# Performance work log

Hardware: AMD Instinct MI355X
Metric: run time of the kernel (lower is better)

## Reference

```python
import jax, jax.numpy as jnp
import numpy as np

B, T, D, H = 2, 2048, 1024, 16
DH = D // H


def setup_inputs() -> dict:
    key = jax.random.key(0)
    ks = jax.random.split(key, 5)
    s = 1.0 / np.sqrt(D)
    return {
        "x": jax.random.normal(ks[0], (B, T, D), dtype=jnp.float32),
        "Wq": jax.random.normal(ks[1], (D, D), dtype=jnp.float32) * s,
        "Wk": jax.random.normal(ks[2], (D, D), dtype=jnp.float32) * s,
        "Wv": jax.random.normal(ks[3], (D, D), dtype=jnp.float32) * s,
        "Wo": jax.random.normal(ks[4], (D, D), dtype=jnp.float32) * s,
    }


def reference(x, Wq, Wk, Wv, Wo):
    # torch nn.Linear(bias=False): y = x @ W.T, weight shape [out, in]
    q = (x @ Wq.T).reshape(B, T, H, DH).transpose(0, 2, 1, 3)  # [B,H,T,Dh]
    k = (x @ Wk.T).reshape(B, T, H, DH).transpose(0, 2, 1, 3)
    v = (x @ Wv.T).reshape(B, T, H, DH).transpose(0, 2, 1, 3)
    scores = jnp.einsum("bhqd,bhkd->bhqk", q, k) / jnp.sqrt(jnp.float32(DH))
    att = jax.nn.softmax(scores, axis=-1)
    y = jnp.einsum("bhqk,bhkd->bhqd", att, v)  # [B,H,T,Dh]
    y = y.transpose(0, 2, 1, 3).reshape(B, T, D)
    return y @ Wo.T
```

## Files before the change

### kernel.cpp

```cpp
#include <hip/hip_runtime.h>
#include <math.h>

typedef __attribute__((ext_vector_type(8))) _Float16 half8;
typedef __attribute__((ext_vector_type(4))) float f32x4;

namespace {
constexpr int T_ = 2048, DH_ = 64;
constexpr int M_ = 4096;
constexpr int KD = 1024;
}

__global__ __launch_bounds__(256)
void conv_half4(const float* __restrict__ s0, const float* __restrict__ s1,
                const float* __restrict__ s2, const float* __restrict__ s3,
                _Float16* __restrict__ dst)
{
    const float* s = (blockIdx.y == 0) ? s0 : (blockIdx.y == 1) ? s1
                   : (blockIdx.y == 2) ? s2 : s3;
    const size_t i = ((size_t)blockIdx.x * 256 + threadIdx.x) * 8;
    const float4 a = *reinterpret_cast<const float4*>(s + i);
    const float4 b = *reinterpret_cast<const float4*>(s + i + 4);
    half8 h;
    h[0] = (_Float16)a.x; h[1] = (_Float16)a.y; h[2] = (_Float16)a.z; h[3] = (_Float16)a.w;
    h[4] = (_Float16)b.x; h[5] = (_Float16)b.y; h[6] = (_Float16)b.z; h[7] = (_Float16)b.w;
    *reinterpret_cast<half8*>(dst + (size_t)blockIdx.y * 1048576 + i) = h;
}

__global__ __launch_bounds__(256)
void gemm_half(const _Float16* __restrict__ A, const _Float16* __restrict__ Bw,
               float* __restrict__ Cout,
               _Float16* __restrict__ qh, _Float16* __restrict__ kh,
               _Float16* __restrict__ vh, const int mode)
{
    __shared__ _Float16 As[128 * 64];
    __shared__ _Float16 Bs[64 * 64];
    const int tid = threadIdx.x;
    const int l   = tid & 63;
    const int w   = tid >> 6;
    const int wm  = w >> 1, wn = w & 1;
    const int m0  = blockIdx.y * 128;
    const int n0  = blockIdx.x * 64;

    f32x4 acc[4][2];
#pragma unroll
    for (int i = 0; i < 4; ++i)
#pragma unroll
        for (int j = 0; j < 2; ++j) acc[i][j] = (f32x4){0.f, 0.f, 0.f, 0.f};

    const int srow = l >> 3;
    const int scol = ((l & 7) ^ srow) << 3;
    const int frow = l & 15;
    const int fkb  = (l >> 4) << 4;

    for (int kt = 0; kt < 16; ++kt) {
        const int kOff = kt << 6;
#pragma unroll
        for (int s = 0; s < 4; ++s) {
            const int j = (w << 2) + s;
            const _Float16* gp = A + (size_t)(m0 + (j << 3) + srow) * KD + kOff + scol;
            __builtin_amdgcn_global_load_lds(
                (const __attribute__((address_space(1))) void*)gp,
                (__attribute__((address_space(3))) void*)(As + (j << 9)), 16, 0, 0);
        }
#pragma unroll
        for (int s = 0; s < 2; ++s) {
            const int j = (w << 1) + s;
            const _Float16* gp = Bw + (size_t)(n0 + (j << 3) + srow) * KD + kOff + scol;
            __builtin_amdgcn_global_load_lds(
                (const __attribute__((address_space(1))) void*)gp,
                (__attribute__((address_space(3))) void*)(Bs + (j << 9)), 16, 0, 0);
        }
        __syncthreads();
#pragma unroll
        for (int ks = 0; ks < 2; ++ks) {
            half8 af[4], bfr[2];
#pragma unroll
            for (int fi = 0; fi < 4; ++fi) {
                const int row = wm * 64 + fi * 16 + frow;
                const int cb  = (ks * 64 + fkb) ^ ((row & 7) << 4);
                af[fi] = *reinterpret_cast<const half8*>(
                    reinterpret_cast<const char*>(As) + row * 128 + cb);
            }
#pragma unroll
            for (int fj = 0; fj < 2; ++fj) {
                const int row = wn * 32 + fj * 16 + frow;
                const int cb  = (ks * 64 + fkb) ^ ((row & 7) << 4);
                bfr[fj] = *reinterpret_cast<const half8*>(
                    reinterpret_cast<const char*>(Bs) + row * 128 + cb);
            }
#pragma unroll
            for (int fi = 0; fi < 4; ++fi)
#pragma unroll
                for (int fj = 0; fj < 2; ++fj)
                    acc[fi][fj] = __builtin_amdgcn_mfma_f32_16x16x32_f16(
                        af[fi], bfr[fj], acc[fi][fj], 0, 0, 0);
        }
        __syncthreads();
    }

    const int r0 = (l >> 4) << 2;
#pragma unroll
    for (int fi = 0; fi < 4; ++fi)
#pragma unroll
        for (int fj = 0; fj < 2; ++fj)
#pragma unroll
            for (int r = 0; r < 4; ++r) {
                const int m = m0 + wm * 64 + fi * 16 + r0 + r;
                const int n = n0 + wn * 32 + fj * 16 + (l & 15);
                const float vv = acc[fi][fj][r];
                if (mode == 0) {
                    const int bb = m >> 11, t = m & 2047;
                    const int which = n >> 10, nl = n & 1023;
                    const int hh = nl >> 6, dh = nl & 63;
                    const int bh = (bb << 4) + hh;
                    if (which == 0)
                        qh[(((size_t)bh << 11) + t) * 64 + dh] = (_Float16)(vv * 0.125f);
                    else if (which == 1)
                        kh[(((size_t)bh << 11) + t) * 64 + dh] = (_Float16)vv;
                    else
                        vh[(((size_t)bh << 6) + dh) * 2048 + t] = (_Float16)vv;
                } else {
                    Cout[(size_t)m * 1024 + n] = vv;
                }
            }
}

#define SWZ(row, bytecol) (((row) << 7) + ((bytecol) ^ (((row) & 7) << 4)))

__global__ __launch_bounds__(256)
void attn_mfma(const _Float16* __restrict__ Qh, const _Float16* __restrict__ Kh,
               const _Float16* __restrict__ Vh, _Float16* __restrict__ Yh)
{
    __shared__ _Float16 Ks[2][64 * 64];
    __shared__ _Float16 Vs[2][64 * 64];
    __shared__ _Float16 Ps[64 * 64];
    const int tid = threadIdx.x;
    const int l   = tid & 63;
    const int w   = tid >> 6;
    const int g4  = l >> 4;
    const int c16 = l & 15;
    const int bh  = blockIdx.y;
    const int t0  = blockIdx.x * 64;
    const size_t qkbase = (size_t)bh * T_ * DH_;
    const size_t vbase  = (size_t)bh * DH_ * T_;

    const int srow = l >> 3;
    const int scol = ((l & 7) ^ srow) << 3;

    half8 qf[2];
#pragma unroll
    for (int ks = 0; ks < 2; ++ks)
        qf[ks] = *reinterpret_cast<const half8*>(
            Qh + qkbase + (size_t)(t0 + w * 16 + c16) * 64 + ks * 32 + g4 * 8);

    half8 ones;
#pragma unroll
    for (int j = 0; j < 8; ++j) ones[j] = (_Float16)1.f;

#pragma unroll
    for (int s = 0; s < 2; ++s) {
        const int j   = (w << 1) + s;
        const int row = (j << 3) + srow;
        const _Float16* gk = Kh + qkbase + (size_t)row * 64 + scol;
        __builtin_amdgcn_global_load_lds(
            (const __attribute__((address_space(1))) void*)gk,
            (__attribute__((address_space(3))) void*)(&Ks[0][0] + (j << 9)), 16, 0, 0);
        const _Float16* gv = Vh + vbase + (size_t)row * T_ + scol;
        __builtin_amdgcn_global_load_lds(
            (const __attribute__((address_space(1))) void*)gv,
            (__attribute__((address_space(3))) void*)(&Vs[0][0] + (j << 9)), 16, 0, 0);
    }
    __syncthreads();

    f32x4 o[4], ol;
#pragma unroll
    for (int i = 0; i < 4; ++i) o[i] = (f32x4){0.f, 0.f, 0.f, 0.f};
    ol = (f32x4){0.f, 0.f, 0.f, 0.f};

    for (int ktile = 0; ktile < T_ / 64; ++ktile) {
        const int cur = ktile & 1;
        if (ktile + 1 < T_ / 64) {
            const int nxt = cur ^ 1;
#pragma unroll
            for (int s = 0; s < 2; ++s) {
                const int j   = (w << 1) + s;
                const int row = (j << 3) + srow;
                const _Float16* gk = Kh + qkbase +
                    (size_t)((ktile + 1) * 64 + row) * 64 + scol;
                __builtin_amdgcn_global_load_lds(
                    (const __attribute__((address_space(1))) void*)gk,
                    (__attribute__((address_space(3))) void*)(&Ks[nxt][0] + (j << 9)), 16, 0, 0);
                const _Float16* gv = Vh + vbase + (size_t)row * T_ +
                    (ktile + 1) * 64 + scol;
                __builtin_amdgcn_global_load_lds(
                    (const __attribute__((address_space(1))) void*)gv,
                    (__attribute__((address_space(3))) void*)(&Vs[nxt][0] + (j << 9)), 16, 0, 0);
            }
        }

        const char* ksBase = reinterpret_cast<const char*>(&Ks[cur][0]);
        const char* vsBase = reinterpret_cast<const char*>(&Vs[cur][0]);
        f32x4 s[4];
#pragma unroll
        for (int fj = 0; fj < 4; ++fj) s[fj] = (f32x4){0.f, 0.f, 0.f, 0.f};
        __builtin_amdgcn_s_setprio(1);
#pragma unroll
        for (int ks = 0; ks < 2; ++ks)
#pragma unroll
            for (int fj = 0; fj < 4; ++fj) {
                const int row = fj * 16 + c16;
                const half8 kf = *reinterpret_cast<const half8*>(
                    ksBase + SWZ(row, ks * 64 + (g4 << 4)));
                s[fj] = __builtin_amdgcn_mfma_f32_16x16x32_f16(qf[ks], kf, s[fj], 0, 0, 0);
            }
        __builtin_amdgcn_s_setprio(0);

#pragma unroll
        for (int r4 = 0; r4 < 4; ++r4) {
            const int q = w * 16 + (g4 << 2) + r4;
#pragma unroll
            for (int fj = 0; fj < 4; ++fj) {
                const float p = __expf(fminf(s[fj][r4], 11.f));
                *reinterpret_cast<_Float16*>(reinterpret_cast<char*>(Ps) +
                    SWZ(q, fj * 32 + (c16 << 1))) = (_Float16)p;
            }
        }

        __builtin_amdgcn_s_setprio(1);
#pragma unroll
        for (int ks = 0; ks < 2; ++ks) {
            const int prow = w * 16 + c16;
            const half8 pf = *reinterpret_cast<const half8*>(
                reinterpret_cast<const char*>(Ps) + SWZ(prow, ks * 64 + (g4 << 4)));
#pragma unroll
            for (int fj = 0; fj < 4; ++fj) {
                const int vrow = fj * 16 + c16;
                const half8 vf = *reinterpret_cast<const half8*>(
                    vsBase + SWZ(vrow, ks * 64 + (g4 << 4)));
                o[fj] = __builtin_amdgcn_mfma_f32_16x16x32_f16(pf, vf, o[fj], 0, 0, 0);
            }
            ol = __builtin_amdgcn_mfma_f32_16x16x32_f16(pf, ones, ol, 0, 0, 0);
        }
        __builtin_amdgcn_s_setprio(0);

        __syncthreads();
    }

    const int bb = bh >> 4, hh = bh & 15;
#pragma unroll
    for (int r4 = 0; r4 < 4; ++r4) {
        const int t = t0 + w * 16 + (g4 << 2) + r4;
        const float inv = 1.f / ol[r4];
        const size_t mrow = ((size_t)bb * T_ + t) * 1024;
#pragma unroll
        for (int fj = 0; fj < 4; ++fj) {
            const int col = hh * 64 + fj * 16 + c16;
            Yh[mrow + col] = (_Float16)(o[fj][r4] * inv);
        }
    }
}

extern "C" void kernel_launch(void* const* d_in, const int* in_sizes, int n_in,
                              void* d_out, int out_size, void* d_ws, size_t ws_size,
                              hipStream_t stream)
{
    const float* x  = (const float*)d_in[0];
    const float* Wq = (const float*)d_in[1];
    const float* Wk = (const float*)d_in[2];
    const float* Wv = (const float*)d_in[3];
    const float* Wo = (const float*)d_in[4];

    unsigned char* ws = (unsigned char*)d_ws;
    _Float16* xh = (_Float16*)ws;
    _Float16* wh = (_Float16*)(ws + (size_t) 8388608);
    _Float16* qh = (_Float16*)(ws + (size_t)16777216);
    _Float16* kh = (_Float16*)(ws + (size_t)25165824);
    _Float16* vh = (_Float16*)(ws + (size_t)33554432);
    _Float16* yh = xh;

    conv_half4<<<dim3(2048, 1), 256, 0, stream>>>(x, nullptr, nullptr, nullptr, xh);
    conv_half4<<<dim3(512, 4), 256, 0, stream>>>(Wq, Wk, Wv, Wo, wh);

    dim3 blk(256);
    dim3 g1(48, 32);
    gemm_half<<<g1, blk, 0, stream>>>(xh, wh, nullptr, qh, kh, vh, 0);

    dim3 ga(T_ / 64, 32);
    attn_mfma<<<ga, blk, 0, stream>>>(qh, kh, vh, yh);

    dim3 g2(16, 32);
    gemm_half<<<g2, blk, 0, stream>>>(yh, wh + (size_t)3072 * KD, (float*)d_out,
                                      nullptr, nullptr, nullptr, 1);
}
```

Before: 154.7 us.

## Enlarge GEMM N-tile to 128 and give each attention warp 32 query rows

The projection GEMMs now compute 128x128 tiles instead of 128x64, so every A-tile load feeds twice as many MFMAs. The attention kernel processes 128 queries per block, with each warp handling two 16-row groups that share each K/V fragment read from LDS. The softmax scale now folds log2(e) into Q so the kernel can use exp2f, with the overflow clamp adjusted to match. In exchange, register pressure rises and there are fewer blocks: 256 for the out-projection and 512 for attention, which may underfill the GPU's compute units.

```diff
diff --git a/kernel.cpp b/kernel.cpp
--- a/kernel.cpp
+++ b/kernel.cpp
@@ -33,19 +33,19 @@
                _Float16* __restrict__ vh, const int mode)
 {
     __shared__ _Float16 As[128 * 64];
-    __shared__ _Float16 Bs[64 * 64];
+    __shared__ _Float16 Bs[128 * 64];
     const int tid = threadIdx.x;
     const int l   = tid & 63;
     const int w   = tid >> 6;
     const int wm  = w >> 1, wn = w & 1;
     const int m0  = blockIdx.y * 128;
-    const int n0  = blockIdx.x * 64;
-
-    f32x4 acc[4][2];
+    const int n0  = blockIdx.x * 128;
+
+    f32x4 acc[4][4];
 #pragma unroll
     for (int i = 0; i < 4; ++i)
 #pragma unroll
-        for (int j = 0; j < 2; ++j) acc[i][j] = (f32x4){0.f, 0.f, 0.f, 0.f};
+        for (int j = 0; j < 4; ++j) acc[i][j] = (f32x4){0.f, 0.f, 0.f, 0.f};
 
     const int srow = l >> 3;
     const int scol = ((l & 7) ^ srow) << 3;
@@ -63,8 +63,8 @@
                 (__attribute__((address_space(3))) void*)(As + (j << 9)), 16, 0, 0);
         }
 #pragma unroll
-        for (int s = 0; s < 2; ++s) {
-            const int j = (w << 1) + s;
+        for (int s = 0; s < 4; ++s) {
+            const int j = (w << 2) + s;
             const _Float16* gp = Bw + (size_t)(n0 + (j << 3) + srow) * KD + kOff + scol;
             __builtin_amdgcn_global_load_lds(
                 (const __attribute__((address_space(1))) void*)gp,
@@ -73,7 +73,7 @@
         __syncthreads();
 #pragma unroll
         for (int ks = 0; ks < 2; ++ks) {
-            half8 af[4], bfr[2];
+            half8 af[4], bfr[4];
 #pragma unroll
             for (int fi = 0; fi < 4; ++fi) {
                 const int row = wm * 64 + fi * 16 + frow;
@@ -82,8 +82,8 @@
                     reinterpret_cast<const char*>(As) + row * 128 + cb);
             }
 #pragma unroll
-            for (int fj = 0; fj < 2; ++fj) {
-                const int row = wn * 32 + fj * 16 + frow;
+            for (int fj = 0; fj < 4; ++fj) {
+                const int row = wn * 64 + fj * 16 + frow;
                 const int cb  = (ks * 64 + fkb) ^ ((row & 7) << 4);
                 bfr[fj] = *reinterpret_cast<const half8*>(
                     reinterpret_cast<const char*>(Bs) + row * 128 + cb);
@@ -91,7 +91,7 @@
 #pragma unroll
             for (int fi = 0; fi < 4; ++fi)
 #pragma unroll
-                for (int fj = 0; fj < 2; ++fj)
+                for (int fj = 0; fj < 4; ++fj)
                     acc[fi][fj] = __builtin_amdgcn_mfma_f32_16x16x32_f16(
                         af[fi], bfr[fj], acc[fi][fj], 0, 0, 0);
         }
@@ -99,14 +99,15 @@
     }
 
     const int r0 = (l >> 4) << 2;
+    const float QSC = 0.125f * 1.44269504f;
 #pragma unroll
     for (int fi = 0; fi < 4; ++fi)
 #pragma unroll
-        for (int fj = 0; fj < 2; ++fj)
+        for (int fj = 0; fj < 4; ++fj)
 #pragma unroll
             for (int r = 0; r < 4; ++r) {
                 const int m = m0 + wm * 64 + fi * 16 + r0 + r;
-                const int n = n0 + wn * 32 + fj * 16 + (l & 15);
+                const int n = n0 + wn * 64 + fj * 16 + (l & 15);
                 const float vv = acc[fi][fj][r];
                 if (mode == 0) {
                     const int bb = m >> 11, t = m & 2047;
@@ -114,7 +115,7 @@
                     const int hh = nl >> 6, dh = nl & 63;
                     const int bh = (bb << 4) + hh;
                     if (which == 0)
-                        qh[(((size_t)bh << 11) + t) * 64 + dh] = (_Float16)(vv * 0.125f);
+                        qh[(((size_t)bh << 11) + t) * 64 + dh] = (_Float16)(vv * QSC);
                     else if (which == 1)
                         kh[(((size_t)bh << 11) + t) * 64 + dh] = (_Float16)vv;
                     else
@@ -133,25 +134,28 @@
 {
     __shared__ _Float16 Ks[2][64 * 64];
     __shared__ _Float16 Vs[2][64 * 64];
-    __shared__ _Float16 Ps[64 * 64];
+    __shared__ _Float16 Ps[128 * 64];
     const int tid = threadIdx.x;
     const int l   = tid & 63;
     const int w   = tid >> 6;
     const int g4  = l >> 4;
     const int c16 = l & 15;
     const int bh  = blockIdx.y;
-    const int t0  = blockIdx.x * 64;
+    const int t0  = blockIdx.x * 128;
     const size_t qkbase = (size_t)bh * T_ * DH_;
     const size_t vbase  = (size_t)bh * DH_ * T_;
 
     const int srow = l >> 3;
     const int scol = ((l & 7) ^ srow) << 3;
 
-    half8 qf[2];
-#pragma unroll
-    for (int ks = 0; ks < 2; ++ks)
-        qf[ks] = *reinterpret_cast<const half8*>(
-            Qh + qkbase + (size_t)(t0 + w * 16 + c16) * 64 + ks * 32 + g4 * 8);
+    half8 qf[2][2];
+#pragma unroll
+    for (int ri = 0; ri < 2; ++ri)
+#pragma unroll
+        for (int ks = 0; ks < 2; ++ks)
+            qf[ri][ks] = *reinterpret_cast<const half8*>(
+                Qh + qkbase + (size_t)(t0 + w * 32 + ri * 16 + c16) * 64
+                    + ks * 32 + g4 * 8);
 
     half8 ones;
 #pragma unroll
@@ -172,10 +176,13 @@
     }
     __syncthreads();
 
-    f32x4 o[4], ol;
-#pragma unroll
-    for (int i = 0; i < 4; ++i) o[i] = (f32x4){0.f, 0.f, 0.f, 0.f};
-    ol = (f32x4){0.f, 0.f, 0.f, 0.f};
+    f32x4 o[2][4], ol[2];
+#pragma unroll
+    for (int ri = 0; ri < 2; ++ri) {
+#pragma unroll
+        for (int i = 0; i < 4; ++i) o[ri][i] = (f32x4){0.f, 0.f, 0.f, 0.f};
+        ol[ri] = (f32x4){0.f, 0.f, 0.f, 0.f};
+    }
 
     for (int ktile = 0; ktile < T_ / 64; ++ktile) {
         const int cur = ktile & 1;
@@ -200,9 +207,11 @@
 
         const char* ksBase = reinterpret_cast<const char*>(&Ks[cur][0]);
         const char* vsBase = reinterpret_cast<const char*>(&Vs[cur][0]);
-        f32x4 s[4];
-#pragma unroll
-        for (int fj = 0; fj < 4; ++fj) s[fj] = (f32x4){0.f, 0.f, 0.f, 0.f};
+        f32x4 s[2][4];
+#pragma unroll
+        for (int ri = 0; ri < 2; ++ri)
+#pragma unroll
+            for (int fj = 0; fj < 4; ++fj) s[ri][fj] = (f32x4){0.f, 0.f, 0.f, 0.f};
         __builtin_amdgcn_s_setprio(1);
 #pragma unroll
         for (int ks = 0; ks < 2; ++ks)
@@ -211,35 +220,41 @@
                 const int row = fj * 16 + c16;
                 const half8 kf = *reinterpret_cast<const half8*>(
                     ksBase + SWZ(row, ks * 64 + (g4 << 4)));
-                s[fj] = __builtin_amdgcn_mfma_f32_16x16x32_f16(qf[ks], kf, s[fj], 0, 0, 0);
+                s[0][fj] = __builtin_amdgcn_mfma_f32_16x16x32_f16(qf[0][ks], kf, s[0][fj], 0, 0, 0);
+                s[1][fj] = __builtin_amdgcn_mfma_f32_16x16x32_f16(qf[1][ks], kf, s[1][fj], 0, 0, 0);
             }
         __builtin_amdgcn_s_setprio(0);
 
 #pragma unroll
-        for (int r4 = 0; r4 < 4; ++r4) {
-            const int q = w * 16 + (g4 << 2) + r4;
-#pragma unroll
-            for (int fj = 0; fj < 4; ++fj) {
-                const float p = __expf(fminf(s[fj][r4], 11.f));
-                *reinterpret_cast<_Float16*>(reinterpret_cast<char*>(Ps) +
-                    SWZ(q, fj * 32 + (c16 << 1))) = (_Float16)p;
-            }
-        }
+        for (int ri = 0; ri < 2; ++ri)
+#pragma unroll
+            for (int r4 = 0; r4 < 4; ++r4) {
+                const int q = w * 32 + ri * 16 + (g4 << 2) + r4;
+#pragma unroll
+                for (int fj = 0; fj < 4; ++fj) {
+                    const float p = exp2f(fminf(s[ri][fj][r4], 15.9f));
+                    *reinterpret_cast<_Float16*>(reinterpret_cast<char*>(Ps) +
+                        SWZ(q, fj * 32 + (c16 << 1))) = (_Float16)p;
+                }
+            }
 
         __builtin_amdgcn_s_setprio(1);
 #pragma unroll
         for (int ks = 0; ks < 2; ++ks) {
-            const int prow = w * 16 + c16;
-            const half8 pf = *reinterpret_cast<const half8*>(
-                reinterpret_cast<const char*>(Ps) + SWZ(prow, ks * 64 + (g4 << 4)));
+            const half8 pf0 = *reinterpret_cast<const half8*>(
+                reinterpret_cast<const char*>(Ps) + SWZ(w * 32 + c16, ks * 64 + (g4 << 4)));
+            const half8 pf1 = *reinterpret_cast<const half8*>(
+                reinterpret_cast<const char*>(Ps) + SWZ(w * 32 + 16 + c16, ks * 64 + (g4 << 4)));
 #pragma unroll
             for (int fj = 0; fj < 4; ++fj) {
                 const int vrow = fj * 16 + c16;
                 const half8 vf = *reinterpret_cast<const half8*>(
                     vsBase + SWZ(vrow, ks * 64 + (g4 << 4)));
-                o[fj] = __builtin_amdgcn_mfma_f32_16x16x32_f16(pf, vf, o[fj], 0, 0, 0);
-            }
-            ol = __builtin_amdgcn_mfma_f32_16x16x32_f16(pf, ones, ol, 0, 0, 0);
+                o[0][fj] = __builtin_amdgcn_mfma_f32_16x16x32_f16(pf0, vf, o[0][fj], 0, 0, 0);
+                o[1][fj] = __builtin_amdgcn_mfma_f32_16x16x32_f16(pf1, vf, o[1][fj], 0, 0, 0);
+            }
+            ol[0] = __builtin_amdgcn_mfma_f32_16x16x32_f16(pf0, ones, ol[0], 0, 0, 0);
+            ol[1] = __builtin_amdgcn_mfma_f32_16x16x32_f16(pf1, ones, ol[1], 0, 0, 0);
         }
         __builtin_amdgcn_s_setprio(0);
 
@@ -248,16 +263,18 @@
 
     const int bb = bh >> 4, hh = bh & 15;
 #pragma unroll
-    for (int r4 = 0; r4 < 4; ++r4) {
-        const int t = t0 + w * 16 + (g4 << 2) + r4;
-        const float inv = 1.f / ol[r4];
-        const size_t mrow = ((size_t)bb * T_ + t) * 1024;
-#pragma unroll
-        for (int fj = 0; fj < 4; ++fj) {
-            const int col = hh * 64 + fj * 16 + c16;
-            Yh[mrow + col] = (_Float16)(o[fj][r4] * inv);
-        }
-    }
+    for (int ri = 0; ri < 2; ++ri)
+#pragma unroll
+        for (int r4 = 0; r4 < 4; ++r4) {
+            const int t = t0 + w * 32 + ri * 16 + (g4 << 2) + r4;
+            const float inv = 1.f / ol[ri][r4];
+            const size_t mrow = ((size_t)bb * T_ + t) * 1024;
+#pragma unroll
+            for (int fj = 0; fj < 4; ++fj) {
+                const int col = hh * 64 + fj * 16 + c16;
+                Yh[mrow + col] = (_Float16)(o[ri][fj][r4] * inv);
+            }
+        }
 }
 
 extern "C" void kernel_launch(void* const* d_in, const int* in_sizes, int n_in,
@@ -282,13 +299,13 @@
     conv_half4<<<dim3(512, 4), 256, 0, stream>>>(Wq, Wk, Wv, Wo, wh);
 
     dim3 blk(256);
-    dim3 g1(48, 32);
+    dim3 g1(24, 32);
     gemm_half<<<g1, blk, 0, stream>>>(xh, wh, nullptr, qh, kh, vh, 0);
 
-    dim3 ga(T_ / 64, 32);
+    dim3 ga(T_ / 128, 32);
     attn_mfma<<<ga, blk, 0, stream>>>(qh, kh, vh, yh);
 
-    dim3 g2(16, 32);
+    dim3 g2(8, 32);
     gemm_half<<<g2, blk, 0, stream>>>(yh, wh + (size_t)3072 * KD, (float*)d_out,
                                       nullptr, nullptr, nullptr, 1);
 }
```

New measurement: 176.7 us. +14.2%, slower.

## Widen QKV GEMM tile to 128 columns and fold log2e into Q scale

Applied to the files above, without the earlier changes.

The GEMM kernel is templated on the N tile width. The QKV projection now uses 128x128 tiles (24x32 grid), halving the number of blocks and increasing data reuse per block, while the output projection keeps 64-wide tiles. Q is additionally pre-scaled by log2(e), so attention can use exp2f instead of __expf, which saves a multiply per score. The clamp is adjusted to 15.9 to keep the fp16 P values in range. Larger tiles mean more accumulator registers and fewer blocks for the GPU to fill its CUs with.

```diff
diff --git a/kernel.cpp b/kernel.cpp
--- a/kernel.cpp
+++ b/kernel.cpp
@@ -26,26 +26,28 @@
     *reinterpret_cast<half8*>(dst + (size_t)blockIdx.y * 1048576 + i) = h;
 }
 
+template <int BN>
 __global__ __launch_bounds__(256)
 void gemm_half(const _Float16* __restrict__ A, const _Float16* __restrict__ Bw,
                float* __restrict__ Cout,
                _Float16* __restrict__ qh, _Float16* __restrict__ kh,
                _Float16* __restrict__ vh, const int mode)
 {
+    constexpr int NF = BN / 32;
     __shared__ _Float16 As[128 * 64];
-    __shared__ _Float16 Bs[64 * 64];
+    __shared__ _Float16 Bs[BN * 64];
     const int tid = threadIdx.x;
     const int l   = tid & 63;
     const int w   = tid >> 6;
     const int wm  = w >> 1, wn = w & 1;
     const int m0  = blockIdx.y * 128;
-    const int n0  = blockIdx.x * 64;
-
-    f32x4 acc[4][2];
+    const int n0  = blockIdx.x * BN;
+
+    f32x4 acc[4][NF];
 #pragma unroll
     for (int i = 0; i < 4; ++i)
 #pragma unroll
-        for (int j = 0; j < 2; ++j) acc[i][j] = (f32x4){0.f, 0.f, 0.f, 0.f};
+        for (int j = 0; j < NF; ++j) acc[i][j] = (f32x4){0.f, 0.f, 0.f, 0.f};
 
     const int srow = l >> 3;
     const int scol = ((l & 7) ^ srow) << 3;
@@ -63,8 +65,8 @@
                 (__attribute__((address_space(3))) void*)(As + (j << 9)), 16, 0, 0);
         }
 #pragma unroll
-        for (int s = 0; s < 2; ++s) {
-            const int j = (w << 1) + s;
+        for (int s = 0; s < BN / 32; ++s) {
+            const int j = w * (BN / 32) + s;
             const _Float16* gp = Bw + (size_t)(n0 + (j << 3) + srow) * KD + kOff + scol;
             __builtin_amdgcn_global_load_lds(
                 (const __attribute__((address_space(1))) void*)gp,
@@ -73,7 +75,7 @@
         __syncthreads();
 #pragma unroll
         for (int ks = 0; ks < 2; ++ks) {
-            half8 af[4], bfr[2];
+            half8 af[4], bfr[NF];
 #pragma unroll
             for (int fi = 0; fi < 4; ++fi) {
                 const int row = wm * 64 + fi * 16 + frow;
@@ -82,8 +84,8 @@
                     reinterpret_cast<const char*>(As) + row * 128 + cb);
             }
 #pragma unroll
-            for (int fj = 0; fj < 2; ++fj) {
-                const int row = wn * 32 + fj * 16 + frow;
+            for (int fj = 0; fj < NF; ++fj) {
+                const int row = wn * (NF * 16) + fj * 16 + frow;
                 const int cb  = (ks * 64 + fkb) ^ ((row & 7) << 4);
                 bfr[fj] = *reinterpret_cast<const half8*>(
                     reinterpret_cast<const char*>(Bs) + row * 128 + cb);
@@ -91,7 +93,7 @@
 #pragma unroll
             for (int fi = 0; fi < 4; ++fi)
 #pragma unroll
-                for (int fj = 0; fj < 2; ++fj)
+                for (int fj = 0; fj < NF; ++fj)
                     acc[fi][fj] = __builtin_amdgcn_mfma_f32_16x16x32_f16(
                         af[fi], bfr[fj], acc[fi][fj], 0, 0, 0);
         }
@@ -99,14 +101,15 @@
     }
 
     const int r0 = (l >> 4) << 2;
+    const float QSC = 0.125f * 1.44269504f;
 #pragma unroll
     for (int fi = 0; fi < 4; ++fi)
 #pragma unroll
-        for (int fj = 0; fj < 2; ++fj)
+        for (int fj = 0; fj < NF; ++fj)
 #pragma unroll
             for (int r = 0; r < 4; ++r) {
                 const int m = m0 + wm * 64 + fi * 16 + r0 + r;
-                const int n = n0 + wn * 32 + fj * 16 + (l & 15);
+                const int n = n0 + wn * (NF * 16) + fj * 16 + (l & 15);
                 const float vv = acc[fi][fj][r];
                 if (mode == 0) {
                     const int bb = m >> 11, t = m & 2047;
@@ -114,7 +117,7 @@
                     const int hh = nl >> 6, dh = nl & 63;
                     const int bh = (bb << 4) + hh;
                     if (which == 0)
-                        qh[(((size_t)bh << 11) + t) * 64 + dh] = (_Float16)(vv * 0.125f);
+                        qh[(((size_t)bh << 11) + t) * 64 + dh] = (_Float16)(vv * QSC);
                     else if (which == 1)
                         kh[(((size_t)bh << 11) + t) * 64 + dh] = (_Float16)vv;
                     else
@@ -220,7 +223,7 @@
             const int q = w * 16 + (g4 << 2) + r4;
 #pragma unroll
             for (int fj = 0; fj < 4; ++fj) {
-                const float p = __expf(fminf(s[fj][r4], 11.f));
+                const float p = exp2f(fminf(s[fj][r4], 15.9f));
                 *reinterpret_cast<_Float16*>(reinterpret_cast<char*>(Ps) +
                     SWZ(q, fj * 32 + (c16 << 1))) = (_Float16)p;
             }
@@ -282,13 +285,13 @@
     conv_half4<<<dim3(512, 4), 256, 0, stream>>>(Wq, Wk, Wv, Wo, wh);
 
     dim3 blk(256);
-    dim3 g1(48, 32);
-    gemm_half<<<g1, blk, 0, stream>>>(xh, wh, nullptr, qh, kh, vh, 0);
+    dim3 g1(24, 32);
+    gemm_half<128><<<g1, blk, 0, stream>>>(xh, wh, nullptr, qh, kh, vh, 0);
 
     dim3 ga(T_ / 64, 32);
     attn_mfma<<<ga, blk, 0, stream>>>(qh, kh, vh, yh);
 
     dim3 g2(16, 32);
-    gemm_half<<<g2, blk, 0, stream>>>(yh, wh + (size_t)3072 * KD, (float*)d_out,
-                                      nullptr, nullptr, nullptr, 1);
-}
+    gemm_half<64><<<g2, blk, 0, stream>>>(yh, wh + (size_t)3072 * KD, (float*)d_out,
+                                          nullptr, nullptr, nullptr, 1);
+}
```

Measured after the change: 167.4 us. 1.08x slower.
